# Performance work log

Measured on AMD Instinct MI355X. Metric: run time of the kernel, lower is better.

## Reference

```python
import jax, jax.numpy as jnp
import numpy as np

D_MODEL = 512
NHEAD = 8
COORD_DIM = 3
B, N = 2, 2048


def setup_inputs() -> dict:
    key = jax.random.key(0)
    ks = jax.random.split(key, 6)
    x = jax.random.normal(ks[0], (B, N, D_MODEL), dtype=jnp.float32)
    coords = jax.random.normal(ks[1], (B, N, COORD_DIM), dtype=jnp.float32)
    attn_mask = jax.random.normal(ks[2], (N, N), dtype=jnp.float32)
    # qkv Linear(d_model, 3*d_model) with bias
    lim = 1.0 / np.sqrt(D_MODEL)
    qkv_w = jax.random.uniform(ks[3], (3 * D_MODEL, D_MODEL), dtype=jnp.float32, minval=-lim, maxval=lim)
    qkv_b = jax.random.uniform(ks[4], (3 * D_MODEL,), dtype=jnp.float32, minval=-lim, maxval=lim)
    # rel_weight is zeros-init in torch; use small random values for a nontrivial test
    rel_weight = 0.02 * jax.random.normal(ks[5], (NHEAD, COORD_DIM), dtype=jnp.float32)
    return {"x": x, "coords": coords, "attn_mask": attn_mask,
            "qkv_w": qkv_w, "qkv_b": qkv_b, "rel_weight": rel_weight}


def reference(x, coords, attn_mask, qkv_w, qkv_b, rel_weight):
    Bb, Nn, D = x.shape
    H = rel_weight.shape[0]
    hd = D // H
    scale = 1.0 / jnp.sqrt(jnp.asarray(hd, dtype=x.dtype))

    qkv = x @ qkv_w.T + qkv_b                      # [B,N,3D]
    q, k, v = jnp.split(qkv, 3, axis=-1)

    def to_heads(t):
        return t.reshape(Bb, Nn, H, hd).transpose(0, 2, 1, 3)  # [B,H,N,hd]

    qh, kh, vh = to_heads(q), to_heads(k), to_heads(v)

    # per-head scalar projection of coordinates: [B,H,N]
    coord_proj = jnp.einsum('bnc,hc->bhn', coords.astype(jnp.float32), rel_weight).astype(x.dtype)

    # scores with relative-coordinate bias and additive float mask (2d kind)
    scores = jnp.einsum('bhqd,bhkd->bhqk', qh, kh) * scale
    scores = scores + coord_proj[:, :, :, None] - coord_proj[:, :, None, :]
    scores = scores + attn_mask[None, None, :, :]

    attn = jax.nn.softmax(scores, axis=-1)
    yh = jnp.einsum('bhqk,bhkd->bhqd', attn, vh)   # [B,H,N,hd]
    return yh.transpose(0, 2, 1, 3).reshape(Bb, Nn, D)
```

## Files before the change

kernel.cpp:

```cpp
#include <hip/hip_runtime.h>
#include <hip/hip_bf16.h>

typedef __bf16 bf16;
typedef __bf16 bf16x4 __attribute__((ext_vector_type(4)));
typedef __bf16 bf16x8 __attribute__((ext_vector_type(8)));
typedef float floatx4 __attribute__((ext_vector_type(4)));

#define D_MODEL 512
#define NHEAD 8
#define HD 64
#define NB 2
#define NN 2048
#define BH (NB*NHEAD)
#define LOG2E 1.4426950408889634f

__global__ __launch_bounds__(256) void convxw(const float* __restrict__ x,
                                              const float* __restrict__ w,
                                              const float* __restrict__ coords,
                                              const float* __restrict__ rw,
                                              bf16* __restrict__ xb,
                                              bf16* __restrict__ wb,
                                              float* __restrict__ cp) {
    int bid = blockIdx.x;
    if (bid >= 2816) {
        int idx = (bid - 2816) * 256 + threadIdx.x;
        int b = idx >> 11, n = idx & 2047;
        float c0 = coords[idx*3 + 0];
        float c1 = coords[idx*3 + 1];
        float c2 = coords[idx*3 + 2];
        for (int h = 0; h < NHEAD; h++) {
            float v = c0*rw[h*3+0] + c1*rw[h*3+1] + c2*rw[h*3+2];
            cp[(size_t)(b*NHEAD + h)*NN + n] = v * LOG2E;
        }
        return;
    }
    int idx = bid * 256 + threadIdx.x;
    const float* src; bf16* dst; int i4;
    if (idx < 524288) { src = x; dst = xb; i4 = idx; }
    else              { src = w; dst = wb; i4 = idx - 524288; }
    float4 v = *(const float4*)(src + (size_t)i4*4);
    bf16x4 o; o[0] = (bf16)v.x; o[1] = (bf16)v.y; o[2] = (bf16)v.z; o[3] = (bf16)v.w;
    *(bf16x4*)(dst + (size_t)i4*4) = o;
}

__global__ __launch_bounds__(256, 4) void qkv_gemm(const bf16* __restrict__ xb,
                                                   const bf16* __restrict__ wb,
                                                   const float* __restrict__ bias,
                                                   bf16* __restrict__ qb,
                                                   bf16* __restrict__ kb,
                                                   bf16* __restrict__ vtb) {
    __shared__ bf16 smem[64*72 + 128*72];
    bf16 (*Ws)[72] = (bf16(*)[72])smem;
    bf16 (*Xs)[72] = (bf16(*)[72])(smem + 64*72);
    int t = threadIdx.x;
    int w = t >> 6, lane = t & 63, quad = lane >> 4, l15 = lane & 15;
    int blk = blockIdx.x;
    int bf = blk % 24, bm = blk / 24;
    int f0 = bf * 64, m0 = bm * 128;

    floatx4 acc[4][2] = {};
    int wrow = t >> 2, wcol = (t & 3) * 16;
    int xrow = t >> 1, xcol = (t & 1) * 32;

    for (int k0 = 0; k0 < D_MODEL; k0 += 64) {
        __syncthreads();
        {
            const bf16* wsrc = wb + (size_t)(f0 + wrow)*D_MODEL + k0 + wcol;
            *(bf16x8*)&Ws[wrow][wcol]   = *(const bf16x8*)wsrc;
            *(bf16x8*)&Ws[wrow][wcol+8] = *(const bf16x8*)(wsrc + 8);
            const bf16* xsrc = xb + (size_t)(m0 + xrow)*D_MODEL + k0 + xcol;
            *(bf16x8*)&Xs[xrow][xcol]    = *(const bf16x8*)xsrc;
            *(bf16x8*)&Xs[xrow][xcol+8]  = *(const bf16x8*)(xsrc + 8);
            *(bf16x8*)&Xs[xrow][xcol+16] = *(const bf16x8*)(xsrc + 16);
            *(bf16x8*)&Xs[xrow][xcol+24] = *(const bf16x8*)(xsrc + 24);
        }
        __syncthreads();
        for (int kf = 0; kf < 2; kf++) {
            bf16x8 af[4], bx[2];
            for (int fi = 0; fi < 4; fi++)
                af[fi] = *(const bf16x8*)&Ws[fi*16 + l15][kf*32 + quad*8];
            for (int mj = 0; mj < 2; mj++)
                bx[mj] = *(const bf16x8*)&Xs[w*32 + mj*16 + l15][kf*32 + quad*8];
            for (int fi = 0; fi < 4; fi++)
                for (int mj = 0; mj < 2; mj++)
                    acc[fi][mj] = __builtin_amdgcn_mfma_f32_16x16x32_bf16(af[fi], bx[mj], acc[fi][mj], 0, 0, 0);
        }
    }

    int mat = f0 >> 9;
    int h = (f0 >> 6) & 7;
    int b = m0 >> 11;
    int nb = m0 & 2047;
    size_t bho = (size_t)(b*NHEAD + h);
    float4 bs4[4];
    for (int fi = 0; fi < 4; fi++)
        bs4[fi] = *(const float4*)(bias + f0 + fi*16 + quad*4);

    if (mat < 2) {
        bf16* dst = (mat == 0) ? qb : kb;
        float sc = (mat == 0) ? 0.125f * LOG2E : 1.0f;
        for (int fi = 0; fi < 4; fi++) {
            for (int mj = 0; mj < 2; mj++) {
                int n = nb + w*32 + mj*16 + l15;
                bf16x4 pv;
                pv[0] = (bf16)((acc[fi][mj][0] + bs4[fi].x) * sc);
                pv[1] = (bf16)((acc[fi][mj][1] + bs4[fi].y) * sc);
                pv[2] = (bf16)((acc[fi][mj][2] + bs4[fi].z) * sc);
                pv[3] = (bf16)((acc[fi][mj][3] + bs4[fi].w) * sc);
                *(bf16x4*)(dst + (bho*NN + n)*HD + fi*16 + quad*4) = pv;
            }
        }
    } else {
        __syncthreads();
        bf16* Vt = smem;
        for (int fi = 0; fi < 4; fi++) {
            int d = fi*16 + quad*4;
            for (int mj = 0; mj < 2; mj++) {
                int mlc = w*32 + mj*16 + l15;
                Vt[(d+0)*136 + mlc] = (bf16)(acc[fi][mj][0] + bs4[fi].x);
                Vt[(d+1)*136 + mlc] = (bf16)(acc[fi][mj][1] + bs4[fi].y);
                Vt[(d+2)*136 + mlc] = (bf16)(acc[fi][mj][2] + bs4[fi].z);
                Vt[(d+3)*136 + mlc] = (bf16)(acc[fi][mj][3] + bs4[fi].w);
            }
        }
        __syncthreads();
        int d = t >> 2, mc = (t & 3) * 32;
        bf16* gdst = vtb + (bho*HD + d)*NN + nb + mc;
        for (int c = 0; c < 4; c++)
            *(bf16x8*)(gdst + c*8) = *(const bf16x8*)&Vt[d*136 + mc + c*8];
    }
}

__global__ __launch_bounds__(256, 4) void attn(const bf16* __restrict__ qb,
                                               const bf16* __restrict__ kb,
                                               const bf16* __restrict__ vtb,
                                               const float* __restrict__ maskf,
                                               const float* __restrict__ cp,
                                               float* __restrict__ op,
                                               float* __restrict__ ml,
                                               float* __restrict__ out,
                                               int ksplit) {
    __shared__ bf16 Ks[64][72];
    __shared__ bf16 Vts[64][72];
    __shared__ bf16 Ps[64][68];
    __shared__ float Cs[2048];
    int t = threadIdx.x;
    int w = t >> 6, lane = t & 63;
    int quad = lane >> 4, l15 = lane & 15;
    int blk = blockIdx.x;
    int bh = blk & 15;
    int rest = blk >> 4;
    int qt = rest & 31, kp = rest >> 5;
    int q0 = qt * 64;
    int nkeys = NN / ksplit;
    int ntiles = nkeys / 64;
    int kbase = kp * nkeys;
    size_t bhoff = (size_t)bh * (NN * HD);

    bf16x8 aq0, aq1;
    {
        const bf16* qp = qb + bhoff + (size_t)(q0 + w*16 + l15)*HD + quad*8;
        aq0 = *(const bf16x8*)(qp);
        aq1 = *(const bf16x8*)(qp + 32);
    }

    float m_i = -1e30f, l_i = 0.f;
    floatx4 o[4] = {};
    int qrow = q0 + w*16 + l15;
    const float* mrow = maskf + (size_t)qrow * NN;
    const float* cpb = cp + (size_t)bh * NN;
    int srow = t >> 2, scol = (t & 3) * 16;

    for (int i = t; i < nkeys; i += 256) Cs[i] = cpb[kbase + i];

    bf16x8 kr0, kr1, vr0, vr1;
    {
        const bf16* ks = kb + bhoff + (size_t)(kbase + srow)*HD + scol;
        kr0 = *(const bf16x8*)ks; kr1 = *(const bf16x8*)(ks + 8);
        const bf16* vs = vtb + bhoff + (size_t)srow*NN + kbase + scol;
        vr0 = *(const bf16x8*)vs; vr1 = *(const bf16x8*)(vs + 8);
    }
    __syncthreads();

    float4 bias4[4];
    for (int j = 0; j < 4; j++) {
        float4 mv = *(const float4*)(mrow + kbase + j*16 + quad*4);
        float4 cv = *(const float4*)&Cs[j*16 + quad*4];
        bias4[j].x = fmaf(mv.x, LOG2E, -cv.x);
        bias4[j].y = fmaf(mv.y, LOG2E, -cv.y);
        bias4[j].z = fmaf(mv.z, LOG2E, -cv.z);
        bias4[j].w = fmaf(mv.w, LOG2E, -cv.w);
    }

    for (int kt = 0; kt < ntiles; kt++) {
        __syncthreads();
        *(bf16x8*)&Ks[srow][scol]      = kr0;
        *(bf16x8*)&Ks[srow][scol + 8]  = kr1;
        *(bf16x8*)&Vts[srow][scol]     = vr0;
        *(bf16x8*)&Vts[srow][scol + 8] = vr1;
        __syncthreads();

        float4 mn4[4];
        bool more = (kt + 1 < ntiles);
        if (more) {
            int kn = kbase + (kt+1)*64;
            const bf16* ks = kb + bhoff + (size_t)(kn + srow)*HD + scol;
            kr0 = *(const bf16x8*)ks; kr1 = *(const bf16x8*)(ks + 8);
            const bf16* vs = vtb + bhoff + (size_t)srow*NN + kn + scol;
            vr0 = *(const bf16x8*)vs; vr1 = *(const bf16x8*)(vs + 8);
            for (int j = 0; j < 4; j++)
                mn4[j] = *(const float4*)(mrow + kn + j*16 + quad*4);
        }

        floatx4 s[4];
        for (int j = 0; j < 4; j++) {
            s[j][0] = bias4[j].x; s[j][1] = bias4[j].y;
            s[j][2] = bias4[j].z; s[j][3] = bias4[j].w;
            bf16x8 ka0 = *(const bf16x8*)&Ks[j*16 + l15][quad*8];
            bf16x8 ka1 = *(const bf16x8*)&Ks[j*16 + l15][32 + quad*8];
            s[j] = __builtin_amdgcn_mfma_f32_16x16x32_bf16(ka0, aq0, s[j], 0, 0, 0);
            s[j] = __builtin_amdgcn_mfma_f32_16x16x32_bf16(ka1, aq1, s[j], 0, 0, 0);
        }

        float mx = s[0][0];
        for (int j = 0; j < 4; j++)
            for (int r = 0; r < 4; r++) mx = fmaxf(mx, s[j][r]);
        mx = fmaxf(mx, __shfl_xor(mx, 16));
        mx = fmaxf(mx, __shfl_xor(mx, 32));

        if (!__all(mx <= m_i)) {
            float mnew = fmaxf(m_i, mx);
            float al = __builtin_amdgcn_exp2f(m_i - mnew);
            l_i *= al;
            float alc[4];
            for (int r = 0; r < 4; r++) alc[r] = __shfl(al, quad*4 + r);
            for (int dj = 0; dj < 4; dj++)
                for (int r = 0; r < 4; r++) o[dj][r] *= alc[r];
            m_i = mnew;
        }

        float rs = 0.f;
        for (int j = 0; j < 4; j++)
            for (int r = 0; r < 4; r++) {
                float p = __builtin_amdgcn_exp2f(s[j][r] - m_i);
                s[j][r] = p;
                rs += p;
            }
        rs += __shfl_xor(rs, 16);
        rs += __shfl_xor(rs, 32);
        l_i += rs;

        for (int j = 0; j < 4; j++) {
            bf16x4 pv;
            pv[0] = (bf16)s[j][0]; pv[1] = (bf16)s[j][1];
            pv[2] = (bf16)s[j][2]; pv[3] = (bf16)s[j][3];
            *(bf16x4*)&Ps[w*16 + l15][j*16 + quad*4] = pv;
        }

        for (int kf2 = 0; kf2 < 2; kf2++) {
            bf16x4 apl = *(const bf16x4*)&Ps[w*16 + l15][kf2*32 + quad*8];
            bf16x4 aph = *(const bf16x4*)&Ps[w*16 + l15][kf2*32 + quad*8 + 4];
            bf16x8 ap;
            ap[0]=apl[0]; ap[1]=apl[1]; ap[2]=apl[2]; ap[3]=apl[3];
            ap[4]=aph[0]; ap[5]=aph[1]; ap[6]=aph[2]; ap[7]=aph[3];
            for (int dj = 0; dj < 4; dj++) {
                bf16x8 bv = *(const bf16x8*)&Vts[dj*16 + l15][kf2*32 + quad*8];
                o[dj] = __builtin_amdgcn_mfma_f32_16x16x32_bf16(ap, bv, o[dj], 0, 0, 0);
            }
        }

        if (more) {
            int knl = (kt+1)*64;
            for (int j = 0; j < 4; j++) {
                float4 cv = *(const float4*)&Cs[knl + j*16 + quad*4];
                bias4[j].x = fmaf(mn4[j].x, LOG2E, -cv.x);
                bias4[j].y = fmaf(mn4[j].y, LOG2E, -cv.y);
                bias4[j].z = fmaf(mn4[j].z, LOG2E, -cv.z);
                bias4[j].w = fmaf(mn4[j].w, LOG2E, -cv.w);
            }
        }
    }

    int b = bh >> 3, h = bh & 7;
    if (ksplit == 1) {
        float lc[4];
        for (int r = 0; r < 4; r++) lc[r] = __shfl(l_i, quad*4 + r);
        for (int dj = 0; dj < 4; dj++) {
            for (int r = 0; r < 4; r++) {
                int n = q0 + w*16 + quad*4 + r;
                out[((size_t)(b*NN + n))*D_MODEL + h*HD + dj*16 + l15] = o[dj][r] / lc[r];
            }
        }
    } else {
        size_t pbase = (size_t)kp * BH * NN;
        for (int dj = 0; dj < 4; dj++) {
            for (int r = 0; r < 4; r++) {
                int n = q0 + w*16 + quad*4 + r;
                op[(pbase + bh*NN + n)*HD + dj*16 + l15] = o[dj][r];
            }
        }
        if (quad == 0) {
            float2 v; v.x = m_i; v.y = l_i;
            *(float2*)(ml + (pbase + (size_t)bh*NN + qrow)*2) = v;
        }
    }
}

__global__ __launch_bounds__(256) void combineN(const float* __restrict__ op,
                                                const float* __restrict__ ml,
                                                float* __restrict__ out,
                                                int ksplit) {
    int idx = blockIdx.x * 256 + threadIdx.x;
    int row = idx >> 4, c4 = (idx & 15) * 4;
    float mstar = -1e30f;
    for (int kp = 0; kp < ksplit; kp++)
        mstar = fmaxf(mstar, ml[((size_t)kp*BH*NN + row)*2]);
    float denom = 0.f;
    float ax = 0.f, ay = 0.f, az = 0.f, aw = 0.f;
    for (int kp = 0; kp < ksplit; kp++) {
        float2 m2 = *(const float2*)(ml + ((size_t)kp*BH*NN + row)*2);
        float wgt = __builtin_amdgcn_exp2f(m2.x - mstar);
        denom += wgt * m2.y;
        float4 ov = *(const float4*)(op + ((size_t)kp*BH*NN + row)*HD + c4);
        ax += wgt*ov.x; ay += wgt*ov.y; az += wgt*ov.z; aw += wgt*ov.w;
    }
    float inv = 1.0f / denom;
    int bh = row >> 11, q = row & 2047;
    int b = bh >> 3, h = bh & 7;
    float4 res; res.x = ax*inv; res.y = ay*inv; res.z = az*inv; res.w = aw*inv;
    *(float4*)(out + ((size_t)(b*NN + q))*D_MODEL + h*HD + c4) = res;
}

extern "C" void kernel_launch(void* const* d_in, const int* in_sizes, int n_in,
                              void* d_out, int out_size, void* d_ws, size_t ws_size,
                              hipStream_t stream) {
    const float* x      = (const float*)d_in[0];
    const float* coords = (const float*)d_in[1];
    const float* amask  = (const float*)d_in[2];
    const float* qkv_w  = (const float*)d_in[3];
    const float* qkv_b  = (const float*)d_in[4];
    const float* rw     = (const float*)d_in[5];
    float* out = (float*)d_out;

    char* ws = (char*)d_ws;
    float* cp  = (float*)(ws + 0);
    bf16*  xb  = (bf16*) (ws + 131072);
    bf16*  wb  = (bf16*) (ws + 4325376);
    bf16*  qb  = (bf16*) (ws + 5898240);
    bf16*  kb  = (bf16*) (ws + 10092544);
    bf16*  vtb = (bf16*) (ws + 14286848);
    float* op  = (float*)(ws + 18481152);

    int split = 1;
    if (ws_size >= 53084160u)      split = 4;
    else if (ws_size >= 35782656u) split = 2;
    float* ml = (float*)(ws + 18481152 + (size_t)split*8388608);

    convxw   <<<dim3(2832), dim3(256), 0, stream>>>(x, qkv_w, coords, rw, xb, wb, cp);
    qkv_gemm <<<dim3(768),  dim3(256), 0, stream>>>(xb, wb, qkv_b, qb, kb, vtb);
    attn     <<<dim3(512*split), dim3(256), 0, stream>>>(qb, kb, vtb, amask, cp, op, ml, out, split);
    if (split > 1)
        combineN<<<dim3(2048), dim3(256), 0, stream>>>(op, ml, out, split);
}
```

Baseline: 149.8 us.

## Load K/V MFMA fragments directly from global memory, dropping LDS staging

The attention kernel no longer stages K and V^T tiles through shared memory. Each wave now loads its MFMA operand fragments straight from global memory (via L2/L1), which removes two block-wide barriers per key tile. The coordinate-bias buffer is sized dynamically to the key-split length, cutting LDS use and possibly raising occupancy. In exchange, all four waves redundantly fetch the same K/V data, so global and cache traffic rises and the register prefetch of the next tile is gone, which exposes load latency.

Measured after the change: 248.1 us. 65.6% more time.

```diff
diff --git a/kernel.cpp b/kernel.cpp
--- a/kernel.cpp
+++ b/kernel.cpp
@@ -140,10 +140,8 @@
                                                float* __restrict__ ml,
                                                float* __restrict__ out,
                                                int ksplit) {
-    __shared__ bf16 Ks[64][72];
-    __shared__ bf16 Vts[64][72];
     __shared__ bf16 Ps[64][68];
-    __shared__ float Cs[2048];
+    extern __shared__ float Cs[];
     int t = threadIdx.x;
     int w = t >> 6, lane = t & 63;
     int quad = lane >> 4, l15 = lane & 15;
@@ -164,22 +162,16 @@
         aq1 = *(const bf16x8*)(qp + 32);
     }
 
+    const bf16* kfrag = kb  + bhoff + (size_t)(kbase + l15)*HD + quad*8;
+    const bf16* vfrag = vtb + bhoff + (size_t)l15*NN + kbase;
+
     float m_i = -1e30f, l_i = 0.f;
     floatx4 o[4] = {};
     int qrow = q0 + w*16 + l15;
     const float* mrow = maskf + (size_t)qrow * NN;
     const float* cpb = cp + (size_t)bh * NN;
-    int srow = t >> 2, scol = (t & 3) * 16;
 
     for (int i = t; i < nkeys; i += 256) Cs[i] = cpb[kbase + i];
-
-    bf16x8 kr0, kr1, vr0, vr1;
-    {
-        const bf16* ks = kb + bhoff + (size_t)(kbase + srow)*HD + scol;
-        kr0 = *(const bf16x8*)ks; kr1 = *(const bf16x8*)(ks + 8);
-        const bf16* vs = vtb + bhoff + (size_t)srow*NN + kbase + scol;
-        vr0 = *(const bf16x8*)vs; vr1 = *(const bf16x8*)(vs + 8);
-    }
     __syncthreads();
 
     float4 bias4[4];
@@ -193,21 +185,10 @@
     }
 
     for (int kt = 0; kt < ntiles; kt++) {
-        __syncthreads();
-        *(bf16x8*)&Ks[srow][scol]      = kr0;
-        *(bf16x8*)&Ks[srow][scol + 8]  = kr1;
-        *(bf16x8*)&Vts[srow][scol]     = vr0;
-        *(bf16x8*)&Vts[srow][scol + 8] = vr1;
-        __syncthreads();
-
         float4 mn4[4];
         bool more = (kt + 1 < ntiles);
         if (more) {
             int kn = kbase + (kt+1)*64;
-            const bf16* ks = kb + bhoff + (size_t)(kn + srow)*HD + scol;
-            kr0 = *(const bf16x8*)ks; kr1 = *(const bf16x8*)(ks + 8);
-            const bf16* vs = vtb + bhoff + (size_t)srow*NN + kn + scol;
-            vr0 = *(const bf16x8*)vs; vr1 = *(const bf16x8*)(vs + 8);
             for (int j = 0; j < 4; j++)
                 mn4[j] = *(const float4*)(mrow + kn + j*16 + quad*4);
         }
@@ -216,10 +197,18 @@
         for (int j = 0; j < 4; j++) {
             s[j][0] = bias4[j].x; s[j][1] = bias4[j].y;
             s[j][2] = bias4[j].z; s[j][3] = bias4[j].w;
-            bf16x8 ka0 = *(const bf16x8*)&Ks[j*16 + l15][quad*8];
-            bf16x8 ka1 = *(const bf16x8*)&Ks[j*16 + l15][32 + quad*8];
+            const bf16* kp0 = kfrag + (size_t)(kt*64 + j*16)*HD;
+            bf16x8 ka0 = *(const bf16x8*)kp0;
+            bf16x8 ka1 = *(const bf16x8*)(kp0 + 32);
             s[j] = __builtin_amdgcn_mfma_f32_16x16x32_bf16(ka0, aq0, s[j], 0, 0, 0);
             s[j] = __builtin_amdgcn_mfma_f32_16x16x32_bf16(ka1, aq1, s[j], 0, 0, 0);
+        }
+
+        bf16x8 vv0[4], vv1[4];
+        for (int dj = 0; dj < 4; dj++) {
+            const bf16* vp = vfrag + (size_t)dj*16*NN + kt*64 + quad*8;
+            vv0[dj] = *(const bf16x8*)vp;
+            vv1[dj] = *(const bf16x8*)(vp + 32);
         }
 
         float mx = s[0][0];
@@ -264,7 +253,7 @@
             ap[0]=apl[0]; ap[1]=apl[1]; ap[2]=apl[2]; ap[3]=apl[3];
             ap[4]=aph[0]; ap[5]=aph[1]; ap[6]=aph[2]; ap[7]=aph[3];
             for (int dj = 0; dj < 4; dj++) {
-                bf16x8 bv = *(const bf16x8*)&Vts[dj*16 + l15][kf2*32 + quad*8];
+                bf16x8 bv = (kf2 == 0) ? vv0[dj] : vv1[dj];
                 o[dj] = __builtin_amdgcn_mfma_f32_16x16x32_bf16(ap, bv, o[dj], 0, 0, 0);
             }
         }
@@ -356,9 +345,11 @@
     else if (ws_size >= 35782656u) split = 2;
     float* ml = (float*)(ws + 18481152 + (size_t)split*8388608);
 
+    size_t dynlds = (size_t)(NN / split) * sizeof(float);
+
     convxw   <<<dim3(2832), dim3(256), 0, stream>>>(x, qkv_w, coords, rw, xb, wb, cp);
     qkv_gemm <<<dim3(768),  dim3(256), 0, stream>>>(xb, wb, qkv_b, qb, kb, vtb);
-    attn     <<<dim3(512*split), dim3(256), 0, stream>>>(qb, kb, vtb, amask, cp, op, ml, out, split);
+    attn     <<<dim3(512*split), dim3(256), dynlds, stream>>>(qb, kb, vtb, amask, cp, op, ml, out, split);
     if (split > 1)
         combineN<<<dim3(2048), dim3(256), 0, stream>>>(op, ml, out, split);
 }
```
